# Optimization experiments

Measured on AMD Instinct MI355X. Metric: run time of the kernel, lower is better.

## Reference

```python
import jax, jax.numpy as jnp
import numpy as np

ROT_ERR_W = 15.0   # weight[0]
TRANS_ERR_W = 100.0  # weight[1]
CONV_ROT = 0.0
CONV_TRANS = 0.0
EPS = 1e-7
SMALL = 1e-4


def _skew(w):
    # w: [..., 3] -> [..., 3, 3]
    z = jnp.zeros_like(w[..., 0])
    r0 = jnp.stack([z, -w[..., 2], w[..., 1]], axis=-1)
    r1 = jnp.stack([w[..., 2], z, -w[..., 0]], axis=-1)
    r2 = jnp.stack([-w[..., 1], w[..., 0], z], axis=-1)
    return jnp.stack([r0, r1, r2], axis=-2)


def _log_se3(R, t):
    # SE(3) log map. R: [...,3,3], t: [...,3] -> (theta, omega[...,3], v[...,3])
    tr = R[..., 0, 0] + R[..., 1, 1] + R[..., 2, 2]
    cos_t = jnp.clip((tr - 1.0) * 0.5, -1.0 + EPS, 1.0 - EPS)
    theta = jnp.arccos(cos_t)
    sin_t = jnp.sin(theta)
    # vee(R - R^T)/2
    w_vee = 0.5 * jnp.stack([
        R[..., 2, 1] - R[..., 1, 2],
        R[..., 0, 2] - R[..., 2, 0],
        R[..., 1, 0] - R[..., 0, 1],
    ], axis=-1)
    small = theta < SMALL
    safe_sin = jnp.where(small, 1.0, sin_t)
    scale = jnp.where(small, 1.0 + theta * theta / 6.0, theta / safe_sin)
    omega = scale[..., None] * w_vee
    # V^{-1} t -> translational twist
    wx = _skew(omega)
    wx2 = jnp.matmul(wx, wx)
    theta2 = jnp.where(small, 1.0, theta * theta)
    A = jnp.where(
        small,
        jnp.full_like(theta, 1.0 / 12.0),
        (1.0 - (theta * sin_t) / (2.0 * (1.0 - cos_t))) / theta2,
    )
    Vinv = jnp.eye(3, dtype=R.dtype) - 0.5 * wx + A[..., None, None] * wx2
    v = jnp.einsum('...ij,...j->...i', Vinv, t)
    return theta, omega, v


def setup_inputs() -> dict:
    key = jax.random.key(0)
    k1, k2, k3, k4 = jax.random.split(key, 4)
    B, H = 2048, 2048  # n_particles x horizon
    return {
        'ee_pos_batch': jax.random.normal(k1, (B, H, 3), jnp.float32),
        'ee_rot_batch': jax.random.normal(k2, (B, H, 3, 3), jnp.float32),
        'ee_goal_pos': jax.random.normal(k3, (3,), jnp.float32),
        'ee_goal_rot': jax.random.normal(k4, (3, 3), jnp.float32),
        'vec_weight': jnp.ones((6,), jnp.float32),
    }


def reference(ee_pos_batch, ee_rot_batch, ee_goal_pos, ee_goal_rot, vec_weight):
    # goal_to_ee = inverse(ee_to_world) * goal_to_world
    Rt = jnp.swapaxes(ee_rot_batch, -1, -2)                 # R_ee^T, [B,H,3,3]
    R_ge = jnp.matmul(Rt, ee_goal_rot)                       # [B,H,3,3]
    t_ge = jnp.einsum('bhij,bhj->bhi', Rt, ee_goal_pos - ee_pos_batch)
    _, omega, v = _log_se3(R_ge, t_ge)
    # squared_l2 NormCost with unit weight
    position_err = jnp.sum(jnp.square(vec_weight[3:6] * v), axis=-1)
    rotation_err = jnp.sum(jnp.square(vec_weight[0:3] * omega), axis=-1)
    rotation_err = jnp.where(rotation_err < CONV_ROT, 0.0, rotation_err)
    position_err = jnp.where(position_err < CONV_TRANS, 0.0, position_err)
    cost = ROT_ERR_W * rotation_err + TRANS_ERR_W * position_err
    return cost, rotation_err, position_err, v, omega
```

## Files before the change

kernel.cpp:

```cpp
#include <hip/hip_runtime.h>


#define BLOCK 256

__global__ __launch_bounds__(BLOCK) void pose_cost_kernel(
    const float* __restrict__ pos,
    const float* __restrict__ rot,
    const float* __restrict__ gpos,
    const float* __restrict__ grot,
    const float* __restrict__ wvec,
    float* __restrict__ out,
    int N)
{
    __shared__ float sR[BLOCK * 9];
    __shared__ float sP[BLOCK * 3];

    const int t = threadIdx.x;
    const int base = blockIdx.x * BLOCK;
    const bool fullBlock = (base + BLOCK) <= N;

    {
        const float* rsrc = rot + (size_t)base * 9;
        const float* psrc = pos + (size_t)base * 3;
        if (fullBlock) {
            #pragma unroll
            for (int k = 0; k < 9; ++k) sR[k * BLOCK + t] = rsrc[k * BLOCK + t];
            #pragma unroll
            for (int k = 0; k < 3; ++k) sP[k * BLOCK + t] = psrc[k * BLOCK + t];
        } else {
            int rem = N - base;
            #pragma unroll
            for (int k = 0; k < 9; ++k) {
                int i = k * BLOCK + t;
                if (i < rem * 9) sR[i] = rsrc[i];
            }
            #pragma unroll
            for (int k = 0; k < 3; ++k) {
                int i = k * BLOCK + t;
                if (i < rem * 3) sP[i] = psrc[i];
            }
        }
    }

    float G[9], g0, g1, g2, w[6];
    #pragma unroll
    for (int k = 0; k < 9; ++k) G[k] = grot[k];
    g0 = gpos[0]; g1 = gpos[1]; g2 = gpos[2];
    #pragma unroll
    for (int k = 0; k < 6; ++k) w[k] = wvec[k];

    __syncthreads();

    const int idx = base + t;
    const bool active = idx < N;

    float cost = 0.f, re = 0.f, pe = 0.f;
    float v0 = 0.f, v1 = 0.f, v2 = 0.f, o0 = 0.f, o1 = 0.f, o2 = 0.f;

    if (active) {
        float R[9];
        #pragma unroll
        for (int k = 0; k < 9; ++k) R[k] = sR[t * 9 + k];
        const float p0 = sP[t * 3 + 0];
        const float p1 = sP[t * 3 + 1];
        const float p2 = sP[t * 3 + 2];

        const float d0 = g0 - p0, d1 = g1 - p1, d2 = g2 - p2;
        const float tq0 = R[0] * d0 + R[3] * d1 + R[6] * d2;
        const float tq1 = R[1] * d0 + R[4] * d1 + R[7] * d2;
        const float tq2 = R[2] * d0 + R[5] * d1 + R[8] * d2;

        float M[9];
        #pragma unroll
        for (int i = 0; i < 3; ++i) {
            #pragma unroll
            for (int j = 0; j < 3; ++j) {
                M[i * 3 + j] = R[0 + i] * G[0 + j] + R[3 + i] * G[3 + j] + R[6 + i] * G[6 + j];
            }
        }

        const float tr = M[0] + M[4] + M[8];
        float cos_t = (tr - 1.0f) * 0.5f;
        cos_t = fminf(fmaxf(cos_t, -1.0f + 1e-7f), 1.0f - 1e-7f);
        const float theta = acosf(cos_t);
        const float sin_t = sinf(theta);

        const float wv0 = 0.5f * (M[7] - M[5]);
        const float wv1 = 0.5f * (M[2] - M[6]);
        const float wv2 = 0.5f * (M[3] - M[1]);

        const bool small = theta < 1e-4f;
        const float th2 = theta * theta;
        const float scale = small ? (1.0f + th2 * (1.0f / 6.0f)) : (theta / sin_t);
        o0 = scale * wv0; o1 = scale * wv1; o2 = scale * wv2;

        const float theta2 = small ? 1.0f : th2;
        const float A = small ? (1.0f / 12.0f)
                              : (1.0f - (theta * sin_t) / (2.0f * (1.0f - cos_t))) / theta2;

        const float cx0 = o1 * tq2 - o2 * tq1;
        const float cx1 = o2 * tq0 - o0 * tq2;
        const float cx2 = o0 * tq1 - o1 * tq0;
        const float odt = o0 * tq0 + o1 * tq1 + o2 * tq2;
        const float on2 = o0 * o0 + o1 * o1 + o2 * o2;
        v0 = tq0 - 0.5f * cx0 + A * (o0 * odt - on2 * tq0);
        v1 = tq1 - 0.5f * cx1 + A * (o1 * odt - on2 * tq1);
        v2 = tq2 - 0.5f * cx2 + A * (o2 * odt - on2 * tq2);

        const float we0 = w[0] * o0, we1 = w[1] * o1, we2 = w[2] * o2;
        const float wp0 = w[3] * v0, wp1 = w[4] * v1, wp2 = w[5] * v2;
        re = we0 * we0 + we1 * we1 + we2 * we2;
        pe = wp0 * wp0 + wp1 * wp1 + wp2 * wp2;
        re = (re < 0.0f) ? 0.0f : re;
        pe = (pe < 0.0f) ? 0.0f : pe;
        cost = 15.0f * re + 100.0f * pe;

        out[idx] = cost;
        out[(size_t)N + idx] = re;
        out[2 * (size_t)N + idx] = pe;
    }

    __syncthreads();
    if (active) {
        sR[t * 3 + 0] = v0;
        sR[t * 3 + 1] = v1;
        sR[t * 3 + 2] = v2;
        sR[BLOCK * 3 + t * 3 + 0] = o0;
        sR[BLOCK * 3 + t * 3 + 1] = o1;
        sR[BLOCK * 3 + t * 3 + 2] = o2;
    }
    __syncthreads();

    {
        float* vdst = out + 3 * (size_t)N + (size_t)base * 3;
        float* odst = out + 6 * (size_t)N + (size_t)base * 3;
        if (fullBlock) {
            #pragma unroll
            for (int k = 0; k < 3; ++k) vdst[k * BLOCK + t] = sR[k * BLOCK + t];
            #pragma unroll
            for (int k = 0; k < 3; ++k) odst[k * BLOCK + t] = sR[BLOCK * 3 + k * BLOCK + t];
        } else {
            int rem = N - base;
            #pragma unroll
            for (int k = 0; k < 3; ++k) {
                int i = k * BLOCK + t;
                if (i < rem * 3) { vdst[i] = sR[i]; odst[i] = sR[BLOCK * 3 + i]; }
            }
        }
    }
}

extern "C" void kernel_launch(void* const* d_in, const int* in_sizes, int n_in,
                              void* d_out, int out_size, void* d_ws, size_t ws_size,
                              hipStream_t stream) {
    const float* pos  = (const float*)d_in[0];
    const float* rot  = (const float*)d_in[1];
    const float* gpos = (const float*)d_in[2];
    const float* grot = (const float*)d_in[3];
    const float* wv   = (const float*)d_in[4];
    float* out = (float*)d_out;

    const int N = in_sizes[0] / 3;
    const int blocks = (N + BLOCK - 1) / BLOCK;
    hipLaunchKernelGGL(pose_cost_kernel, dim3(blocks), dim3(BLOCK), 0, stream,
                       pos, rot, gpos, grot, wv, out, N);
}
```

Before: 295.4 us.

## Process four poses per thread with direct float4 loads and stores

Drops the shared-memory staging and both block barriers. Each thread now processes four consecutive poses, reading them with float4 global loads and writing every output with float4 stores. It also replaces sinf(acos(c)) with sqrt(1-c^2). The cost is uncoalesced per-lane strides (each lane reads 144 contiguous bytes), more registers, and a quarter as many threads.

```diff
diff --git a/kernel.cpp b/kernel.cpp
--- a/kernel.cpp
+++ b/kernel.cpp
@@ -2,6 +2,70 @@
 
 
 #define BLOCK 256
+#define PPT 4
+
+struct PoseOut { float cost, re, pe, v0, v1, v2, o0, o1, o2; };
+
+__device__ __forceinline__ PoseOut pose_compute(
+    const float* __restrict__ R,
+    float p0, float p1, float p2,
+    const float* __restrict__ G,
+    float g0, float g1, float g2,
+    const float* __restrict__ w)
+{
+    PoseOut r;
+    const float d0 = g0 - p0, d1 = g1 - p1, d2 = g2 - p2;
+    const float tq0 = R[0] * d0 + R[3] * d1 + R[6] * d2;
+    const float tq1 = R[1] * d0 + R[4] * d1 + R[7] * d2;
+    const float tq2 = R[2] * d0 + R[5] * d1 + R[8] * d2;
+
+    float M[9];
+    #pragma unroll
+    for (int i = 0; i < 3; ++i)
+        #pragma unroll
+        for (int j = 0; j < 3; ++j)
+            M[i * 3 + j] = R[0 + i] * G[0 + j] + R[3 + i] * G[3 + j] + R[6 + i] * G[6 + j];
+
+    const float tr = M[0] + M[4] + M[8];
+    float cos_t = (tr - 1.0f) * 0.5f;
+    cos_t = fminf(fmaxf(cos_t, -1.0f + 1e-7f), 1.0f - 1e-7f);
+    const float theta = acosf(cos_t);
+    const float sin_t = sqrtf(fmaxf(1.0f - cos_t * cos_t, 0.0f));
+
+    const float wv0 = 0.5f * (M[7] - M[5]);
+    const float wv1 = 0.5f * (M[2] - M[6]);
+    const float wv2 = 0.5f * (M[3] - M[1]);
+
+    const bool small = theta < 1e-4f;
+    const float th2 = theta * theta;
+    const float scale = small ? (1.0f + th2 * (1.0f / 6.0f)) : (theta / sin_t);
+    const float o0 = scale * wv0, o1 = scale * wv1, o2 = scale * wv2;
+
+    const float theta2 = small ? 1.0f : th2;
+    const float A = small ? (1.0f / 12.0f)
+                          : (1.0f - (theta * sin_t) / (2.0f * (1.0f - cos_t))) / theta2;
+
+    const float cx0 = o1 * tq2 - o2 * tq1;
+    const float cx1 = o2 * tq0 - o0 * tq2;
+    const float cx2 = o0 * tq1 - o1 * tq0;
+    const float odt = o0 * tq0 + o1 * tq1 + o2 * tq2;
+    const float on2 = o0 * o0 + o1 * o1 + o2 * o2;
+    const float v0 = tq0 - 0.5f * cx0 + A * (o0 * odt - on2 * tq0);
+    const float v1 = tq1 - 0.5f * cx1 + A * (o1 * odt - on2 * tq1);
+    const float v2 = tq2 - 0.5f * cx2 + A * (o2 * odt - on2 * tq2);
+
+    const float we0 = w[0] * o0, we1 = w[1] * o1, we2 = w[2] * o2;
+    const float wp0 = w[3] * v0, wp1 = w[4] * v1, wp2 = w[5] * v2;
+    float re = we0 * we0 + we1 * we1 + we2 * we2;
+    float pe = wp0 * wp0 + wp1 * wp1 + wp2 * wp2;
+    re = (re < 0.0f) ? 0.0f : re;
+    pe = (pe < 0.0f) ? 0.0f : pe;
+    r.cost = 15.0f * re + 100.0f * pe;
+    r.re = re; r.pe = pe;
+    r.v0 = v0; r.v1 = v1; r.v2 = v2;
+    r.o0 = o0; r.o1 = o1; r.o2 = o2;
+    return r;
+}
 
 __global__ __launch_bounds__(BLOCK) void pose_cost_kernel(
     const float* __restrict__ pos,
@@ -10,37 +74,11 @@
     const float* __restrict__ grot,
     const float* __restrict__ wvec,
     float* __restrict__ out,
-    int N)
+    int N, int vecOK)
 {
-    __shared__ float sR[BLOCK * 9];
-    __shared__ float sP[BLOCK * 3];
-
-    const int t = threadIdx.x;
-    const int base = blockIdx.x * BLOCK;
-    const bool fullBlock = (base + BLOCK) <= N;
-
-    {
-        const float* rsrc = rot + (size_t)base * 9;
-        const float* psrc = pos + (size_t)base * 3;
-        if (fullBlock) {
-            #pragma unroll
-            for (int k = 0; k < 9; ++k) sR[k * BLOCK + t] = rsrc[k * BLOCK + t];
-            #pragma unroll
-            for (int k = 0; k < 3; ++k) sP[k * BLOCK + t] = psrc[k * BLOCK + t];
-        } else {
-            int rem = N - base;
-            #pragma unroll
-            for (int k = 0; k < 9; ++k) {
-                int i = k * BLOCK + t;
-                if (i < rem * 9) sR[i] = rsrc[i];
-            }
-            #pragma unroll
-            for (int k = 0; k < 3; ++k) {
-                int i = k * BLOCK + t;
-                if (i < rem * 3) sP[i] = psrc[i];
-            }
-        }
-    }
+    const int j = blockIdx.x * BLOCK + threadIdx.x;
+    const int p0 = j * PPT;
+    if (p0 >= N) return;
 
     float G[9], g0, g1, g2, w[6];
     #pragma unroll
@@ -49,103 +87,66 @@
     #pragma unroll
     for (int k = 0; k < 6; ++k) w[k] = wvec[k];
 
-    __syncthreads();
-
-    const int idx = base + t;
-    const bool active = idx < N;
-
-    float cost = 0.f, re = 0.f, pe = 0.f;
-    float v0 = 0.f, v1 = 0.f, v2 = 0.f, o0 = 0.f, o1 = 0.f, o2 = 0.f;
-
-    if (active) {
-        float R[9];
-        #pragma unroll
-        for (int k = 0; k < 9; ++k) R[k] = sR[t * 9 + k];
-        const float p0 = sP[t * 3 + 0];
-        const float p1 = sP[t * 3 + 1];
-        const float p2 = sP[t * 3 + 2];
-
-        const float d0 = g0 - p0, d1 = g1 - p1, d2 = g2 - p2;
-        const float tq0 = R[0] * d0 + R[3] * d1 + R[6] * d2;
-        const float tq1 = R[1] * d0 + R[4] * d1 + R[7] * d2;
-        const float tq2 = R[2] * d0 + R[5] * d1 + R[8] * d2;
-
-        float M[9];
-        #pragma unroll
-        for (int i = 0; i < 3; ++i) {
+    if (vecOK && (p0 + PPT) <= N) {
+        float Rf[36], Pf[12];
+        {
+            const float4* r4 = (const float4*)(rot + (size_t)p0 * 9);
             #pragma unroll
-            for (int j = 0; j < 3; ++j) {
-                M[i * 3 + j] = R[0 + i] * G[0 + j] + R[3 + i] * G[3 + j] + R[6 + i] * G[6 + j];
+            for (int k = 0; k < 9; ++k) {
+                const float4 x = r4[k];
+                Rf[4 * k + 0] = x.x; Rf[4 * k + 1] = x.y;
+                Rf[4 * k + 2] = x.z; Rf[4 * k + 3] = x.w;
+            }
+            const float4* pp = (const float4*)(pos + (size_t)p0 * 3);
+            #pragma unroll
+            for (int k = 0; k < 3; ++k) {
+                const float4 x = pp[k];
+                Pf[4 * k + 0] = x.x; Pf[4 * k + 1] = x.y;
+                Pf[4 * k + 2] = x.z; Pf[4 * k + 3] = x.w;
             }
         }
 
-        const float tr = M[0] + M[4] + M[8];
-        float cos_t = (tr - 1.0f) * 0.5f;
-        cos_t = fminf(fmaxf(cos_t, -1.0f + 1e-7f), 1.0f - 1e-7f);
-        const float theta = acosf(cos_t);
-        const float sin_t = sinf(theta);
+        float c[4], re[4], pe[4], vv[12], oo[12];
+        #pragma unroll
+        for (int q = 0; q < PPT; ++q) {
+            PoseOut o = pose_compute(&Rf[9 * q], Pf[3 * q + 0], Pf[3 * q + 1], Pf[3 * q + 2],
+                                     G, g0, g1, g2, w);
+            c[q] = o.cost; re[q] = o.re; pe[q] = o.pe;
+            vv[3 * q + 0] = o.v0; vv[3 * q + 1] = o.v1; vv[3 * q + 2] = o.v2;
+            oo[3 * q + 0] = o.o0; oo[3 * q + 1] = o.o1; oo[3 * q + 2] = o.o2;
+        }
 
-        const float wv0 = 0.5f * (M[7] - M[5]);
-        const float wv1 = 0.5f * (M[2] - M[6]);
-        const float wv2 = 0.5f * (M[3] - M[1]);
-
-        const bool small = theta < 1e-4f;
-        const float th2 = theta * theta;
-        const float scale = small ? (1.0f + th2 * (1.0f / 6.0f)) : (theta / sin_t);
-        o0 = scale * wv0; o1 = scale * wv1; o2 = scale * wv2;
-
-        const float theta2 = small ? 1.0f : th2;
-        const float A = small ? (1.0f / 12.0f)
-                              : (1.0f - (theta * sin_t) / (2.0f * (1.0f - cos_t))) / theta2;
-
-        const float cx0 = o1 * tq2 - o2 * tq1;
-        const float cx1 = o2 * tq0 - o0 * tq2;
-        const float cx2 = o0 * tq1 - o1 * tq0;
-        const float odt = o0 * tq0 + o1 * tq1 + o2 * tq2;
-        const float on2 = o0 * o0 + o1 * o1 + o2 * o2;
-        v0 = tq0 - 0.5f * cx0 + A * (o0 * odt - on2 * tq0);
-        v1 = tq1 - 0.5f * cx1 + A * (o1 * odt - on2 * tq1);
-        v2 = tq2 - 0.5f * cx2 + A * (o2 * odt - on2 * tq2);
-
-        const float we0 = w[0] * o0, we1 = w[1] * o1, we2 = w[2] * o2;
-        const float wp0 = w[3] * v0, wp1 = w[4] * v1, wp2 = w[5] * v2;
-        re = we0 * we0 + we1 * we1 + we2 * we2;
-        pe = wp0 * wp0 + wp1 * wp1 + wp2 * wp2;
-        re = (re < 0.0f) ? 0.0f : re;
-        pe = (pe < 0.0f) ? 0.0f : pe;
-        cost = 15.0f * re + 100.0f * pe;
-
-        out[idx] = cost;
-        out[(size_t)N + idx] = re;
-        out[2 * (size_t)N + idx] = pe;
-    }
-
-    __syncthreads();
-    if (active) {
-        sR[t * 3 + 0] = v0;
-        sR[t * 3 + 1] = v1;
-        sR[t * 3 + 2] = v2;
-        sR[BLOCK * 3 + t * 3 + 0] = o0;
-        sR[BLOCK * 3 + t * 3 + 1] = o1;
-        sR[BLOCK * 3 + t * 3 + 2] = o2;
-    }
-    __syncthreads();
-
-    {
-        float* vdst = out + 3 * (size_t)N + (size_t)base * 3;
-        float* odst = out + 6 * (size_t)N + (size_t)base * 3;
-        if (fullBlock) {
+        *(float4*)(out + p0)                 = make_float4(c[0], c[1], c[2], c[3]);
+        *(float4*)(out + (size_t)N + p0)     = make_float4(re[0], re[1], re[2], re[3]);
+        *(float4*)(out + 2 * (size_t)N + p0) = make_float4(pe[0], pe[1], pe[2], pe[3]);
+        float* vdst = out + 3 * (size_t)N + (size_t)p0 * 3;
+        float* odst = out + 6 * (size_t)N + (size_t)p0 * 3;
+        #pragma unroll
+        for (int k = 0; k < 3; ++k) {
+            *(float4*)(vdst + 4 * k) = make_float4(vv[4 * k], vv[4 * k + 1], vv[4 * k + 2], vv[4 * k + 3]);
+            *(float4*)(odst + 4 * k) = make_float4(oo[4 * k], oo[4 * k + 1], oo[4 * k + 2], oo[4 * k + 3]);
+        }
+    } else {
+        #pragma unroll
+        for (int q = 0; q < PPT; ++q) {
+            const int i = p0 + q;
+            if (i >= N) break;
+            float R[9];
             #pragma unroll
-            for (int k = 0; k < 3; ++k) vdst[k * BLOCK + t] = sR[k * BLOCK + t];
-            #pragma unroll
-            for (int k = 0; k < 3; ++k) odst[k * BLOCK + t] = sR[BLOCK * 3 + k * BLOCK + t];
-        } else {
-            int rem = N - base;
-            #pragma unroll
-            for (int k = 0; k < 3; ++k) {
-                int i = k * BLOCK + t;
-                if (i < rem * 3) { vdst[i] = sR[i]; odst[i] = sR[BLOCK * 3 + i]; }
-            }
+            for (int k = 0; k < 9; ++k) R[k] = rot[(size_t)i * 9 + k];
+            const float pp0 = pos[(size_t)i * 3 + 0];
+            const float pp1 = pos[(size_t)i * 3 + 1];
+            const float pp2 = pos[(size_t)i * 3 + 2];
+            PoseOut o = pose_compute(R, pp0, pp1, pp2, G, g0, g1, g2, w);
+            out[i] = o.cost;
+            out[(size_t)N + i] = o.re;
+            out[2 * (size_t)N + i] = o.pe;
+            out[3 * (size_t)N + (size_t)i * 3 + 0] = o.v0;
+            out[3 * (size_t)N + (size_t)i * 3 + 1] = o.v1;
+            out[3 * (size_t)N + (size_t)i * 3 + 2] = o.v2;
+            out[6 * (size_t)N + (size_t)i * 3 + 0] = o.o0;
+            out[6 * (size_t)N + (size_t)i * 3 + 1] = o.o1;
+            out[6 * (size_t)N + (size_t)i * 3 + 2] = o.o2;
         }
     }
 }
@@ -161,7 +162,9 @@
     float* out = (float*)d_out;
 
     const int N = in_sizes[0] / 3;
-    const int blocks = (N + BLOCK - 1) / BLOCK;
+    const int vecOK = (N % 4 == 0) ? 1 : 0;
+    const int threads_needed = (N + PPT - 1) / PPT;
+    const int blocks = (threads_needed + BLOCK - 1) / BLOCK;
     hipLaunchKernelGGL(pose_cost_kernel, dim3(blocks), dim3(BLOCK), 0, stream,
-                       pos, rot, gpos, grot, wv, out, N);
+                       pos, rot, gpos, grot, wv, out, N, vecOK);
 }
```

After: 302.3 us. 1.02x slower.
